# Performance work log

Measured on AMD Instinct MI355X. Metric: run time of the kernel, lower is better.

Reference implementation:

```python
import jax, jax.numpy as jnp
import numpy as np

B, S, D, H = 8, 8192, 256, 256


def setup_inputs() -> dict:
    key = jax.random.key(0)
    ks = jax.random.split(key, 5)
    scale = 1.0 / np.sqrt(D)  # mimic nn.Linear init scale
    return {
        "x": jax.random.normal(ks[0], (B, S, D), dtype=jnp.float32),
        "h0": jnp.zeros((B, 1, H), dtype=jnp.float32),
        "w_h_w": jax.random.normal(ks[1], (H, D), dtype=jnp.float32) * scale,
        "w_h_b": jax.random.normal(ks[2], (H,), dtype=jnp.float32) * scale,
        "w_z_w": jax.random.normal(ks[3], (H, D), dtype=jnp.float32) * scale,
        "w_z_b": jax.random.normal(ks[4], (H,), dtype=jnp.float32) * scale,
    }


def reference(x, h0, w_h_w, w_h_b, w_z_w, w_z_b):
    # Projections over the whole sequence (same math as per-step Linear calls)
    z = jax.nn.sigmoid(jnp.einsum('bsd,hd->bsh', x, w_z_w) + w_z_b)  # [B,S,H]
    h_tilde = jnp.einsum('bsd,hd->bsh', x, w_h_w) + w_h_b            # [B,S,H]

    def step(h_prev, zh):
        z_t, ht_t = zh  # each [B,H]
        h_t = (1.0 - z_t) * h_prev + z_t * ht_t
        return h_t, h_t

    # scan over time axis; carry is [B,H]
    _, hs = jax.lax.scan(step, h0[:, 0],
                         (jnp.swapaxes(z, 0, 1), jnp.swapaxes(h_tilde, 0, 1)))
    return jnp.swapaxes(hs, 0, 1)  # [B,S,H]
```

## Files before the change

kernel.cpp:

```cpp
#include <hip/hip_runtime.h>
#include <math.h>


constexpr int B_ = 8;
constexpr int S_ = 8192;
constexpr int D_ = 256;
constexpr int H_ = 256;
constexpr int M_ = B_ * S_;
constexpr int CHUNKS = 128;
constexpr int CLEN = S_ / CHUNKS;

typedef __attribute__((ext_vector_type(8))) short bf16x8;
typedef __attribute__((ext_vector_type(4))) float f32x4;

__device__ __forceinline__ uint pack2bf(float f0, float f1) {
  const uint u0 = __float_as_uint(f0) + 0x8000u;
  const uint u1 = __float_as_uint(f1) + 0x8000u;
  return __builtin_amdgcn_perm(u1, u0, 0x07060302u);
}

__global__ __launch_bounds__(256) void gemm_zh(
    const float* __restrict__ x,
    const float* __restrict__ whw, const float* __restrict__ whb,
    const float* __restrict__ wzw, const float* __restrict__ wzb,
    uint* __restrict__ ab, float2* __restrict__ chunkPQ)
{
  __shared__ ushort xs[128][72];
  __shared__ ushort wzs[64][72];
  __shared__ ushort whs[64][72];

  const int tid = threadIdx.x;
  const int g    = blockIdx.x;
  const int xcd  = g & 7;
  const int loc  = g >> 3;
  const int nt   = loc & 3;
  const int panel = (loc >> 2) * 8 + xcd;
  const int m0 = panel * 128;
  const int n0 = nt * 64;

  const int lane = tid & 63;
  const int w  = tid >> 6;
  const int mb = (w & 1) * 64;
  const int nb = (w >> 1) * 32;
  const int q  = lane >> 4;
  const int cn = lane & 15;

  f32x4 accz[4][2] = {};
  f32x4 acch[4][2] = {};

  for (int k0 = 0; k0 < D_; k0 += 64) {
    __syncthreads();
#pragma unroll
    for (int f = 0; f < 8; f++) {
      const int idx = tid + 256 * f;
      const int row = idx >> 4, seg = idx & 15;
      float4 v = *(const float4*)(x + (size_t)(m0 + row) * D_ + k0 + seg * 4);
      *(uint2*)&xs[row][seg * 4] =
          make_uint2(pack2bf(v.x, v.y), pack2bf(v.z, v.w));
    }
#pragma unroll
    for (int f = 0; f < 4; f++) {
      const int idx = tid + 256 * f;
      const int row = idx >> 4, seg = idx & 15;
      float4 vz = *(const float4*)(wzw + (size_t)(n0 + row) * D_ + k0 + seg * 4);
      float4 vh = *(const float4*)(whw + (size_t)(n0 + row) * D_ + k0 + seg * 4);
      *(uint2*)&wzs[row][seg * 4] =
          make_uint2(pack2bf(vz.x, vz.y), pack2bf(vz.z, vz.w));
      *(uint2*)&whs[row][seg * 4] =
          make_uint2(pack2bf(vh.x, vh.y), pack2bf(vh.z, vh.w));
    }
    __syncthreads();
#pragma unroll
    for (int ks = 0; ks < 2; ks++) {
      const int kk = ks * 32 + q * 8;
      bf16x8 af[4], bz[2], bh[2];
#pragma unroll
      for (int i = 0; i < 4; i++)
        af[i] = *(const bf16x8*)&xs[mb + i * 16 + cn][kk];
#pragma unroll
      for (int j = 0; j < 2; j++) {
        bz[j] = *(const bf16x8*)&wzs[nb + j * 16 + cn][kk];
        bh[j] = *(const bf16x8*)&whs[nb + j * 16 + cn][kk];
      }
#pragma unroll
      for (int i = 0; i < 4; i++)
#pragma unroll
        for (int j = 0; j < 2; j++) {
          accz[i][j] = __builtin_amdgcn_mfma_f32_16x16x32_bf16(af[i], bz[j], accz[i][j], 0, 0, 0);
          acch[i][j] = __builtin_amdgcn_mfma_f32_16x16x32_bf16(af[i], bh[j], acch[i][j], 0, 0, 0);
        }
    }
  }

  const int row0 = m0 + mb;
  const int bb2  = row0 >> 13;
  const int cc   = (row0 & 8191) >> 6;

#pragma unroll
  for (int j = 0; j < 2; j++) {
    const int ch = n0 + nb + j * 16 + cn;
    const float zb = wzb[ch], hb = whb[ch];
    uint u[4][4];
#pragma unroll
    for (int i = 0; i < 4; i++) {
#pragma unroll
      for (int r = 0; r < 4; r++) {
        const int row = m0 + mb + i * 16 + q * 4 + r;
        const float zpre = accz[i][j][r] + zb;
        const float hpre = acch[i][j][r] + hb;
        const float e = __expf(-zpre);
        const float rcp = __builtin_amdgcn_rcpf(1.0f + e);
        const uint pk = pack2bf(e * rcp, hpre * rcp);
        ab[(size_t)row * H_ + ch] = pk;
        u[i][r] = pk;
      }
    }
    float P[4], Q[4];
#pragma unroll
    for (int i = 0; i < 4; i++) {
      float Pi = 1.f, Qi = 0.f;
#pragma unroll
      for (int r = 0; r < 4; r++) {
        const float a  = __uint_as_float(u[i][r] << 16);
        const float bv = __uint_as_float(u[i][r] & 0xFFFF0000u);
        Qi = fmaf(a, Qi, bv);
        Pi *= a;
      }
      P[i] = Pi; Q[i] = Qi;
    }
#pragma unroll
    for (int i = 0; i < 4; i++) {
      {
        const float Pp = __shfl_xor(P[i], 16);
        const float Qp = __shfl_xor(Q[i], 16);
        const bool later = (lane & 16) != 0;
        Q[i] = later ? fmaf(P[i], Qp, Q[i]) : fmaf(Pp, Q[i], Qp);
        P[i] = P[i] * Pp;
      }
      {
        const float Pp = __shfl_xor(P[i], 32);
        const float Qp = __shfl_xor(Q[i], 32);
        const bool later = (lane & 32) != 0;
        Q[i] = later ? fmaf(P[i], Qp, Q[i]) : fmaf(Pp, Q[i], Qp);
        P[i] = P[i] * Pp;
      }
    }
    float Pc = P[0], Qc = Q[0];
#pragma unroll
    for (int i = 1; i < 4; i++) {
      Qc = fmaf(P[i], Qc, Q[i]);
      Pc *= P[i];
    }
    if (lane < 16)
      chunkPQ[((size_t)bb2 * CHUNKS + cc) * H_ + ch] = make_float2(Pc, Qc);
  }
}

__global__ __launch_bounds__(256) void scan_phaseB(
    const float* __restrict__ h0in, const float2* __restrict__ pq,
    float* __restrict__ hstate)
{
  const int b = blockIdx.x;
  const int h = threadIdx.x;
  const size_t base = (size_t)b * CHUNKS * H_ + h;
  float hc = h0in[(size_t)b * H_ + h];
  for (int c0 = 0; c0 < CHUNKS; c0 += 16) {
    float2 v[16];
#pragma unroll
    for (int j = 0; j < 16; j++)
      v[j] = pq[base + (size_t)(c0 + j) * H_];
#pragma unroll
    for (int j = 0; j < 16; j++) {
      hstate[base + (size_t)(c0 + j) * H_] = hc;
      hc = fmaf(v[j].x, hc, v[j].y);
    }
  }
}

__global__ __launch_bounds__(256) void scan_phaseC(
    const uint* __restrict__ ab, const float* __restrict__ hstate,
    float* __restrict__ out)
{
  const int c = blockIdx.x;
  const int b = blockIdx.y;
  const int ch = threadIdx.x;
  size_t base = ((size_t)b * S_ + (size_t)c * CLEN) * H_ + ch;
  float hc = hstate[((size_t)b * CHUNKS + c) * H_ + ch];
#pragma unroll
  for (int t0 = 0; t0 < CLEN; t0 += 16) {
    uint v[16];
#pragma unroll
    for (int j = 0; j < 16; j++)
      v[j] = ab[base + (size_t)(t0 + j) * H_];
#pragma unroll
    for (int j = 0; j < 16; j++) {
      const float a  = __uint_as_float(v[j] << 16);
      const float bb = __uint_as_float(v[j] & 0xFFFF0000u);
      hc = fmaf(a, hc, bb);
      out[base + (size_t)(t0 + j) * H_] = hc;
    }
  }
}

extern "C" void kernel_launch(void* const* d_in, const int* in_sizes, int n_in,
                              void* d_out, int out_size, void* d_ws, size_t ws_size,
                              hipStream_t stream) {
  const float* x   = (const float*)d_in[0];
  const float* h0  = (const float*)d_in[1];
  const float* whw = (const float*)d_in[2];
  const float* whb = (const float*)d_in[3];
  const float* wzw = (const float*)d_in[4];
  const float* wzb = (const float*)d_in[5];
  float* out = (float*)d_out;

  uint*   ab      = (uint*)d_ws;
  float2* chunkPQ = (float2*)(ab + (size_t)M_ * H_);
  float*  hstate  = (float*)(chunkPQ + (size_t)B_ * CHUNKS * H_);

  gemm_zh<<<(M_ / 128) * 4, 256, 0, stream>>>(x, whw, whb, wzw, wzb, ab, chunkPQ);
  scan_phaseB<<<B_, 256, 0, stream>>>(h0, (const float2*)chunkPQ, hstate);
  scan_phaseC<<<dim3(CHUNKS, B_), 256, 0, stream>>>(ab, hstate, out);
}
```

Measured before the change: 181.9 us.

## Prepack weight MFMA fragments and refine scan into 16-step subchunks

Adds a prep kernel that converts both weight matrices to bf16 once, laid out in MFMA fragment order. The GEMM then reads B operands straight from global/L2 instead of restaging them through shared memory every k-step, which cuts LDS traffic and per-block weight conversion. The chunk scan now emits four sub-chunk (P,Q) pairs per 64-row chunk, and phase B writes the carried state back into the same buffer in place. Phase C uses 16-step subchunks, with each thread handling 4 channels through uint4/float4 accesses, shortening the serial dependency chain. The cost is a longer phase B scan, an extra launch, and weight fragments fetched from global memory rather than LDS.

```diff
diff --git a/kernel.cpp b/kernel.cpp
--- a/kernel.cpp
+++ b/kernel.cpp
@@ -8,7 +8,8 @@
 constexpr int H_ = 256;
 constexpr int M_ = B_ * S_;
 constexpr int CHUNKS = 128;
-constexpr int CLEN = S_ / CHUNKS;
+constexpr int SUBS = CHUNKS * 4;
+constexpr int WF_U4 = 2 * 16 * 4 * 2 * 4 * 16;
 
 typedef __attribute__((ext_vector_type(8))) short bf16x8;
 typedef __attribute__((ext_vector_type(4))) float f32x4;
@@ -19,15 +20,37 @@
   return __builtin_amdgcn_perm(u1, u0, 0x07060302u);
 }
 
+__device__ __forceinline__ float a_of(uint u) { return __uint_as_float(u << 16); }
+__device__ __forceinline__ float b_of(uint u) { return __uint_as_float(u & 0xFFFF0000u); }
+
+__global__ __launch_bounds__(256) void prep_wfrag(
+    const float* __restrict__ wzw, const float* __restrict__ whw,
+    uint4* __restrict__ wf)
+{
+  const int u = blockIdx.x * 256 + threadIdx.x;
+  const int cn   = u & 15;
+  const int q    = (u >> 4) & 3;
+  const int ks   = (u >> 6) & 1;
+  const int k0b  = (u >> 7) & 3;
+  const int ncg  = (u >> 9) & 15;
+  const int proj = u >> 13;
+  const float* w = proj ? whw : wzw;
+  const float* src = w + (size_t)(ncg * 16 + cn) * D_ + k0b * 64 + ks * 32 + q * 8;
+  uint4 r;
+  r.x = pack2bf(src[0], src[1]);
+  r.y = pack2bf(src[2], src[3]);
+  r.z = pack2bf(src[4], src[5]);
+  r.w = pack2bf(src[6], src[7]);
+  wf[u] = r;
+}
+
 __global__ __launch_bounds__(256) void gemm_zh(
     const float* __restrict__ x,
-    const float* __restrict__ whw, const float* __restrict__ whb,
-    const float* __restrict__ wzw, const float* __restrict__ wzb,
-    uint* __restrict__ ab, float2* __restrict__ chunkPQ)
+    const float* __restrict__ whb, const float* __restrict__ wzb,
+    const uint4* __restrict__ wf,
+    uint* __restrict__ ab, float2* __restrict__ pq)
 {
   __shared__ ushort xs[128][72];
-  __shared__ ushort wzs[64][72];
-  __shared__ ushort whs[64][72];
 
   const int tid = threadIdx.x;
   const int g    = blockIdx.x;
@@ -45,29 +68,22 @@
   const int q  = lane >> 4;
   const int cn = lane & 15;
 
+  const uint4* wfz = wf;
+  const uint4* wfh = wf + (WF_U4 / 2);
+  const int ncg0 = nt * 4 + (w >> 1) * 2;
+
   f32x4 accz[4][2] = {};
   f32x4 acch[4][2] = {};
 
-  for (int k0 = 0; k0 < D_; k0 += 64) {
+  for (int k0b = 0; k0b < 4; k0b++) {
     __syncthreads();
 #pragma unroll
     for (int f = 0; f < 8; f++) {
       const int idx = tid + 256 * f;
       const int row = idx >> 4, seg = idx & 15;
-      float4 v = *(const float4*)(x + (size_t)(m0 + row) * D_ + k0 + seg * 4);
+      float4 v = *(const float4*)(x + (size_t)(m0 + row) * D_ + k0b * 64 + seg * 4);
       *(uint2*)&xs[row][seg * 4] =
           make_uint2(pack2bf(v.x, v.y), pack2bf(v.z, v.w));
-    }
-#pragma unroll
-    for (int f = 0; f < 4; f++) {
-      const int idx = tid + 256 * f;
-      const int row = idx >> 4, seg = idx & 15;
-      float4 vz = *(const float4*)(wzw + (size_t)(n0 + row) * D_ + k0 + seg * 4);
-      float4 vh = *(const float4*)(whw + (size_t)(n0 + row) * D_ + k0 + seg * 4);
-      *(uint2*)&wzs[row][seg * 4] =
-          make_uint2(pack2bf(vz.x, vz.y), pack2bf(vz.z, vz.w));
-      *(uint2*)&whs[row][seg * 4] =
-          make_uint2(pack2bf(vh.x, vh.y), pack2bf(vh.z, vh.w));
     }
     __syncthreads();
 #pragma unroll
@@ -79,8 +95,9 @@
         af[i] = *(const bf16x8*)&xs[mb + i * 16 + cn][kk];
 #pragma unroll
       for (int j = 0; j < 2; j++) {
-        bz[j] = *(const bf16x8*)&wzs[nb + j * 16 + cn][kk];
-        bh[j] = *(const bf16x8*)&whs[nb + j * 16 + cn][kk];
+        const int o = (((ncg0 + j) * 4 + k0b) * 2 + ks) * 64 + lane;
+        bz[j] = *(const bf16x8*)&wfz[o];
+        bh[j] = *(const bf16x8*)&wfh[o];
       }
 #pragma unroll
       for (int i = 0; i < 4; i++)
@@ -121,8 +138,8 @@
       float Pi = 1.f, Qi = 0.f;
 #pragma unroll
       for (int r = 0; r < 4; r++) {
-        const float a  = __uint_as_float(u[i][r] << 16);
-        const float bv = __uint_as_float(u[i][r] & 0xFFFF0000u);
+        const float a  = a_of(u[i][r]);
+        const float bv = b_of(u[i][r]);
         Qi = fmaf(a, Qi, bv);
         Pi *= a;
       }
@@ -145,59 +162,63 @@
         P[i] = P[i] * Pp;
       }
     }
-    float Pc = P[0], Qc = Q[0];
-#pragma unroll
-    for (int i = 1; i < 4; i++) {
-      Qc = fmaf(P[i], Qc, Q[i]);
-      Pc *= P[i];
-    }
-    if (lane < 16)
-      chunkPQ[((size_t)bb2 * CHUNKS + cc) * H_ + ch] = make_float2(Pc, Qc);
+    if (lane < 16) {
+#pragma unroll
+      for (int i = 0; i < 4; i++)
+        pq[((size_t)bb2 * SUBS + cc * 4 + i) * H_ + ch] = make_float2(P[i], Q[i]);
+    }
   }
 }
 
 __global__ __launch_bounds__(256) void scan_phaseB(
-    const float* __restrict__ h0in, const float2* __restrict__ pq,
-    float* __restrict__ hstate)
+    const float* __restrict__ h0in, float2* __restrict__ pq)
 {
   const int b = blockIdx.x;
   const int h = threadIdx.x;
-  const size_t base = (size_t)b * CHUNKS * H_ + h;
+  float2* base = pq + (size_t)b * SUBS * H_ + h;
   float hc = h0in[(size_t)b * H_ + h];
-  for (int c0 = 0; c0 < CHUNKS; c0 += 16) {
-    float2 v[16];
-#pragma unroll
-    for (int j = 0; j < 16; j++)
-      v[j] = pq[base + (size_t)(c0 + j) * H_];
-#pragma unroll
-    for (int j = 0; j < 16; j++) {
-      hstate[base + (size_t)(c0 + j) * H_] = hc;
+  for (int c0 = 0; c0 < SUBS; c0 += 32) {
+    float2 v[32];
+#pragma unroll
+    for (int j = 0; j < 32; j++)
+      v[j] = base[(size_t)(c0 + j) * H_];
+#pragma unroll
+    for (int j = 0; j < 32; j++) {
+      *(float*)&base[(size_t)(c0 + j) * H_] = hc;
       hc = fmaf(v[j].x, hc, v[j].y);
     }
   }
 }
 
 __global__ __launch_bounds__(256) void scan_phaseC(
-    const uint* __restrict__ ab, const float* __restrict__ hstate,
+    const uint* __restrict__ ab, const float2* __restrict__ pq,
     float* __restrict__ out)
 {
   const int c = blockIdx.x;
   const int b = blockIdx.y;
-  const int ch = threadIdx.x;
-  size_t base = ((size_t)b * S_ + (size_t)c * CLEN) * H_ + ch;
-  float hc = hstate[((size_t)b * CHUNKS + c) * H_ + ch];
-#pragma unroll
-  for (int t0 = 0; t0 < CLEN; t0 += 16) {
-    uint v[16];
-#pragma unroll
-    for (int j = 0; j < 16; j++)
-      v[j] = ab[base + (size_t)(t0 + j) * H_];
-#pragma unroll
-    for (int j = 0; j < 16; j++) {
-      const float a  = __uint_as_float(v[j] << 16);
-      const float bb = __uint_as_float(v[j] & 0xFFFF0000u);
-      hc = fmaf(a, hc, bb);
-      out[base + (size_t)(t0 + j) * H_] = hc;
+  const int gq  = threadIdx.x >> 6;
+  const int c64 = threadIdx.x & 63;
+  const int ch4 = c64 * 4;
+  const int sub = c * 4 + gq;
+  const size_t ebase = ((size_t)b * S_ + (size_t)sub * 16) * H_ + ch4;
+
+  const float2* hs = pq + ((size_t)b * SUBS + sub) * H_ + ch4;
+  float h0v = hs[0].x, h1v = hs[1].x, h2v = hs[2].x, h3v = hs[3].x;
+
+#pragma unroll
+  for (int half = 0; half < 2; half++) {
+    uint4 v[8];
+#pragma unroll
+    for (int j = 0; j < 8; j++)
+      v[j] = *(const uint4*)(ab + ebase + (size_t)(half * 8 + j) * H_);
+#pragma unroll
+    for (int j = 0; j < 8; j++) {
+      float4 o;
+      o.x = h0v = fmaf(a_of(v[j].x), h0v, b_of(v[j].x));
+      o.y = h1v = fmaf(a_of(v[j].y), h1v, b_of(v[j].y));
+      o.z = h2v = fmaf(a_of(v[j].z), h2v, b_of(v[j].z));
+      o.w = h3v = fmaf(a_of(v[j].w), h3v, b_of(v[j].w));
+      *(float4*)(out + ebase + (size_t)(half * 8 + j) * H_) = o;
     }
   }
 }
@@ -213,11 +234,12 @@
   const float* wzb = (const float*)d_in[5];
   float* out = (float*)d_out;
 
-  uint*   ab      = (uint*)d_ws;
-  float2* chunkPQ = (float2*)(ab + (size_t)M_ * H_);
-  float*  hstate  = (float*)(chunkPQ + (size_t)B_ * CHUNKS * H_);
-
-  gemm_zh<<<(M_ / 128) * 4, 256, 0, stream>>>(x, whw, whb, wzw, wzb, ab, chunkPQ);
-  scan_phaseB<<<B_, 256, 0, stream>>>(h0, (const float2*)chunkPQ, hstate);
-  scan_phaseC<<<dim3(CHUNKS, B_), 256, 0, stream>>>(ab, hstate, out);
-}
+  uint*   ab = (uint*)d_ws;
+  float2* pq = (float2*)(ab + (size_t)M_ * H_);
+  uint4*  wf = (uint4*)(pq + (size_t)B_ * SUBS * H_);
+
+  prep_wfrag<<<WF_U4 / 256, 256, 0, stream>>>(wzw, whw, wf);
+  gemm_zh<<<(M_ / 128) * 4, 256, 0, stream>>>(x, whb, wzb, wf, ab, pq);
+  scan_phaseB<<<B_, 256, 0, stream>>>(h0, pq);
+  scan_phaseC<<<dim3(CHUNKS, B_), 256, 0, stream>>>(ab, pq, out);
+}
```

Measured after the change: 215.5 us. 18.4% more time.
